# Performance work log

Hardware: AMD Instinct MI355X
Metric: run time of the kernel (lower is better)

The kernel has to match this reference:

```python
import jax, jax.numpy as jnp
import numpy as np

B, T, N, D = 16, 24, 2048, 64
L, K = 2, 3  # num_layers, cheb_k


def setup_inputs() -> dict:
    key = jax.random.key(0)
    ks = jax.random.split(key, 6)
    x = jax.random.normal(ks[0], (B, T, N, D), dtype=jnp.float32)
    init_state = jnp.zeros((L, B, N, D), dtype=jnp.float32)
    adj = jax.random.uniform(ks[1], (N, N), dtype=jnp.float32)
    adj = adj / jnp.sum(adj, axis=-1, keepdims=True)  # row-normalized adjacency
    cin = 2 * D
    Wg = jax.random.normal(ks[2], (L, K, cin, 2 * D), dtype=jnp.float32) * (1.0 / np.sqrt(K * cin))
    bg = jnp.zeros((L, 2 * D), dtype=jnp.float32)
    Wu = jax.random.normal(ks[3], (L, K, cin, D), dtype=jnp.float32) * (1.0 / np.sqrt(K * cin))
    bu = jnp.zeros((L, D), dtype=jnp.float32)
    return {"x": x, "init_state": init_state, "adj_matrix": adj,
            "Wg": Wg, "bg": bg, "Wu": Wu, "bu": bu}


def _cheb_supports(adj, k):
    # T0=I, T1=A, Tk = 2*A@T_{k-1} - T_{k-2}
    n = adj.shape[0]
    sup = [jnp.eye(n, dtype=adj.dtype), adj]
    for _ in range(2, k):
        sup.append(2.0 * adj @ sup[-1] - sup[-2])
    return jnp.stack(sup[:k], axis=0)  # [K, N, N]


def _gconv(xs, supports, W, b):
    # xs: [B,N,Cin], supports: [K,N,N], W: [K,Cin,Cout]
    xg = jnp.einsum('knm,bmc->bknc', supports, xs)
    return jnp.einsum('bknc,kco->bno', xg, W) + b


def _cell(x_t, state, supports, Wg_l, bg_l, Wu_l, bu_l):
    ins = jnp.concatenate([x_t, state], axis=-1)  # [B,N,2D]
    zr = jax.nn.sigmoid(_gconv(ins, supports, Wg_l, bg_l))
    z, r = jnp.split(zr, 2, axis=-1)
    cand_in = jnp.concatenate([x_t, z * state], axis=-1)
    hc = jnp.tanh(_gconv(cand_in, supports, Wu_l, bu_l))
    return r * state + (1.0 - r) * hc


def reference(x, init_state, adj_matrix, Wg, bg, Wu, bu):
    supports = _cheb_supports(adj_matrix, K)
    current = x  # [B,T,N,D]
    hiddens = []
    for l in range(L):
        def step(state, x_t, l=l):
            new = _cell(x_t, state, supports, Wg[l], bg[l], Wu[l], bu[l])
            return new, new
        last, seq = jax.lax.scan(step, init_state[l], jnp.swapaxes(current, 0, 1))
        hiddens.append(last)
        current = x + jnp.swapaxes(seq, 0, 1)  # residual over the stacked states
    return current, jnp.stack(hiddens, axis=0)
```

## Files before the change

### kernel.cpp

```cpp
#include <hip/hip_runtime.h>
#include <hip/hip_bf16.h>
#include <math.h>

typedef __bf16 bf16x8 __attribute__((ext_vector_type(8)));
typedef float f32x4 __attribute__((ext_vector_type(4)));
typedef __hip_bfloat16 bf16s;

constexpr int kB = 16, kT = 24, kN = 2048, kD = 64;
constexpr size_t kBND = (size_t)kB * kN * kD;

struct Slot { const void* p0; const void* p1; int astr0, trow0, astr1, trow1, type; };
struct Slots6 { Slot s[6]; };
struct DiffGrp { const bf16s* src; bf16s* oA; bf16s* oA2; };
struct DiffP { const bf16s* S0; const bf16s* S1; DiffGrp g[4]; int colsPerGrp; };

__device__ __forceinline__ void async_copy16(void* lds, const void* g) {
  __builtin_amdgcn_global_load_lds((const __attribute__((address_space(1))) void*)g,
                                   (__attribute__((address_space(3))) void*)lds,
                                   16, 0, 0);
}


__device__ __forceinline__ void diff_core(
    const bf16s* __restrict__ S, const bf16s* __restrict__ Bsrc,
    int m0, int c0, bf16s* lA, bf16s* lB, f32x4 (&acc)[4][4])
{
  const int tid = threadIdx.x, lane = tid & 63, wave = tid >> 6;
  const int wm = (wave >> 1) * 64, wn = (wave & 1) * 64;
  const f32x4 zero = {0.f, 0.f, 0.f, 0.f};
#pragma unroll
  for (int i = 0; i < 4; ++i)
#pragma unroll
    for (int j = 0; j < 4; ++j) acc[i][j] = zero;

  const int ra = tid >> 3;
  const int cs = ((tid & 7) ^ (ra & 7)) * 8;
  const int rk0 = ((lane >> 4) ^ (lane & 7)) * 8;
  const int rk1 = ((4 + (lane >> 4)) ^ (lane & 7)) * 8;

  for (int k0 = 0; k0 < 2048; k0 += 64) {
#pragma unroll
    for (int i = 0; i < 4; ++i) {
      async_copy16(lA + (size_t)(i * 256 + tid) * 8,
                   S + (size_t)(m0 + i * 32 + ra) * 2048 + k0 + cs);
      async_copy16(lB + (size_t)(i * 256 + tid) * 8,
                   Bsrc + (size_t)(c0 + i * 32 + ra) * 2048 + k0 + cs);
    }
    __syncthreads();
#pragma unroll
    for (int ks = 0; ks < 2; ++ks) {
      const int rk = ks ? rk1 : rk0;
      bf16x8 av[4], bv[4];
#pragma unroll
      for (int f = 0; f < 4; ++f) {
        av[f] = *(const bf16x8*)(lA + (size_t)(wm + f * 16 + (lane & 15)) * 64 + rk);
        bv[f] = *(const bf16x8*)(lB + (size_t)(wn + f * 16 + (lane & 15)) * 64 + rk);
      }
#pragma unroll
      for (int i = 0; i < 4; ++i)
#pragma unroll
        for (int j = 0; j < 4; ++j)
          acc[i][j] = __builtin_amdgcn_mfma_f32_16x16x32_bf16(av[i], bv[j], acc[i][j], 0, 0, 0);
    }
    __syncthreads();
  }
}

__global__ __launch_bounds__(256) void k_diff(DiffP p)
{
  __shared__ bf16s lA[128 * 64];
  __shared__ bf16s lB[128 * 64];
  const int mi = blockIdx.x;
  const bf16s* S = (mi >> 4) ? p.S1 : p.S0;
  const int m0 = (mi & 15) * 128;
  const int ybpg = p.colsPerGrp >> 7;
  const int grp = blockIdx.y / ybpg;
  const int c0 = (blockIdx.y - grp * ybpg) * 128;
  const DiffGrp G = p.g[grp];

  f32x4 acc[4][4];
  diff_core(S, G.src, m0, c0, lA, lB, acc);

  bf16s* out = (mi >> 4) ? G.oA2 : G.oA;
  const int lane = threadIdx.x & 63, wave = threadIdx.x >> 6;
  const int wm = (wave >> 1) * 64, wn = (wave & 1) * 64;
  const int rq = (lane >> 4) * 4, cl = lane & 15;
#pragma unroll
  for (int fm = 0; fm < 4; ++fm)
#pragma unroll
    for (int fn = 0; fn < 4; ++fn)
#pragma unroll
      for (int q = 0; q < 4; ++q) {
        int gm = m0 + wm + fm * 16 + rq + q;
        int gc = c0 + wn + fn * 16 + cl;
        size_t off = ((size_t)(gc >> 6) * 2048 + gm) * 64 + (gc & 63);
        out[off] = __float2bfloat16(acc[fm][fn][q]);
      }
}

__global__ __launch_bounds__(256) void k_a2(
    const bf16s* __restrict__ A, const bf16s* __restrict__ AT, bf16s* A2)
{
  __shared__ bf16s lA[128 * 64];
  __shared__ bf16s lB[128 * 64];
  const int m0 = blockIdx.x * 128, n0 = blockIdx.y * 128;
  f32x4 acc[4][4];
  diff_core(A, AT, m0, n0, lA, lB, acc);
  const int lane = threadIdx.x & 63, wave = threadIdx.x >> 6;
  const int wm = (wave >> 1) * 64, wn = (wave & 1) * 64;
  const int rq = (lane >> 4) * 4, cl = lane & 15;
#pragma unroll
  for (int fm = 0; fm < 4; ++fm)
#pragma unroll
    for (int fn = 0; fn < 4; ++fn)
#pragma unroll
      for (int q = 0; q < 4; ++q) {
        int gm = m0 + wm + fm * 16 + rq + q;
        int gc = n0 + wn + fn * 16 + cl;
        A2[(size_t)gm * 2048 + gc] = __float2bfloat16(2.f * acc[fm][fn][q] - (gm == gc ? 1.f : 0.f));
      }
}

template<int BN>
__device__ __forceinline__ void small_core(
    const Slots6& sl, int m0, const bf16s* __restrict__ W,
    bf16s* lA, bf16s* lB, f32x4 (&acc)[4][BN / 32])
{
  const int tid = threadIdx.x, lane = tid & 63, wave = tid >> 6;
  const int wm = (wave >> 1) * 64, wn = (wave & 1) * (BN / 2);
  const f32x4 zero = {0.f, 0.f, 0.f, 0.f};
#pragma unroll
  for (int i = 0; i < 4; ++i)
#pragma unroll
    for (int j = 0; j < BN / 32; ++j) acc[i][j] = zero;

  const int ra = tid >> 3;
  const int cs = ((tid & 7) ^ (ra & 7)) * 8;
  const int rk0 = ((lane >> 4) ^ (lane & 7)) * 8;
  const int rk1 = ((4 + (lane >> 4)) ^ (lane & 7)) * 8;

#pragma unroll
  for (int ks = 0; ks < 6; ++ks) {
    const Slot sd = sl.s[ks];
    if (sd.type == 0) {
      const bf16s* base = (const bf16s*)sd.p0;
#pragma unroll
      for (int i = 0; i < 4; ++i) {
        int row = m0 + i * 32 + ra;
        size_t roff = ((size_t)(row >> 11) * sd.astr0 + sd.trow0 + (row & 2047)) * 64 + cs;
        async_copy16(lA + (size_t)(i * 256 + tid) * 8, base + roff);
      }
    } else if (sd.type == 1) {
#pragma unroll
      for (int i = 0; i < 4; ++i) {
        int row = m0 + i * 32 + ra;
        size_t roff = ((size_t)(row >> 11) * sd.astr0 + sd.trow0 + (row & 2047)) * 64 + cs;
        const float4* q0 = (const float4*)((const float*)sd.p0 + roff);
        float4 a = q0[0], b = q0[1];
        union { bf16x8 v; bf16s h[8]; } u;
        u.h[0] = __float2bfloat16(a.x); u.h[1] = __float2bfloat16(a.y);
        u.h[2] = __float2bfloat16(a.z); u.h[3] = __float2bfloat16(a.w);
        u.h[4] = __float2bfloat16(b.x); u.h[5] = __float2bfloat16(b.y);
        u.h[6] = __float2bfloat16(b.z); u.h[7] = __float2bfloat16(b.w);
        *(bf16x8*)(lA + (size_t)(i * 256 + tid) * 8) = u.v;
      }
    } else {
#pragma unroll
      for (int i = 0; i < 4; ++i) {
        int row = m0 + i * 32 + ra;
        size_t r0o = ((size_t)(row >> 11) * sd.astr0 + sd.trow0 + (row & 2047)) * 64 + cs;
        size_t r1o = ((size_t)(row >> 11) * sd.astr1 + sd.trow1 + (row & 2047)) * 64 + cs;
        union { bf16x8 v; bf16s h[8]; } a, b, o;
        a.v = *(const bf16x8*)((const bf16s*)sd.p0 + r0o);
        b.v = *(const bf16x8*)((const bf16s*)sd.p1 + r1o);
#pragma unroll
        for (int j = 0; j < 8; ++j)
          o.h[j] = __float2bfloat16(__bfloat162float(a.h[j]) + __bfloat162float(b.h[j]));
        *(bf16x8*)(lA + (size_t)(i * 256 + tid) * 8) = o.v;
      }
    }
#pragma unroll
    for (int i = 0; i < BN / 32; ++i)
      async_copy16(lB + (size_t)(i * 256 + tid) * 8,
                   W + (size_t)(i * 32 + ra) * 384 + ks * 64 + cs);
    __syncthreads();
#pragma unroll
    for (int kss = 0; kss < 2; ++kss) {
      const int rk = kss ? rk1 : rk0;
      bf16x8 av[4], bv[BN / 32];
#pragma unroll
      for (int f = 0; f < 4; ++f)
        av[f] = *(const bf16x8*)(lA + (size_t)(wm + f * 16 + (lane & 15)) * 64 + rk);
#pragma unroll
      for (int f = 0; f < BN / 32; ++f)
        bv[f] = *(const bf16x8*)(lB + (size_t)(wn + f * 16 + (lane & 15)) * 64 + rk);
#pragma unroll
      for (int i = 0; i < 4; ++i)
#pragma unroll
        for (int j = 0; j < BN / 32; ++j)
          acc[i][j] = __builtin_amdgcn_mfma_f32_16x16x32_bf16(av[i], bv[j], acc[i][j], 0, 0, 0);
    }
    __syncthreads();
  }
}

struct LayerG {
  Slots6 sl; const bf16s* W; const float* bias;
  const float* h; bf16s* zh; bf16s* zhT; float* r;
};
__global__ __launch_bounds__(256) void k_gate(LayerG A, LayerG B, int nA)
{
  __shared__ bf16s lA[128 * 64];
  __shared__ bf16s lB[128 * 64];
  const int bx = blockIdx.x;
  const bool isA = bx < nA;
  const LayerG L = isA ? A : B;
  const int m0 = (isA ? bx : bx - nA) * 128;
  f32x4 acc[4][4];
  small_core<128>(L.sl, m0, L.W, lA, lB, acc);
  const int lane = threadIdx.x & 63, wave = threadIdx.x >> 6;
  const int wm = (wave >> 1) * 64, wn = (wave & 1) * 64;
  const int rq = (lane >> 4) * 4, cl = lane & 15;
#pragma unroll
  for (int fm = 0; fm < 4; ++fm)
#pragma unroll
    for (int fn = 0; fn < 4; ++fn) {
      const int o = wn + fn * 16 + cl;
      const float bias = L.bias[o];
#pragma unroll
      for (int q = 0; q < 4; ++q) {
        size_t gm = (size_t)m0 + wm + fm * 16 + rq + q;
        float s = 1.f / (1.f + expf(-(acc[fm][fn][q] + bias)));
        if (o < 64) {
          float zh = s * L.h[gm * 64 + o];
          L.zh[gm * 64 + o] = __float2bfloat16(zh);
          L.zhT[((size_t)((gm >> 11) * 64 + o)) * 2048 + (gm & 2047)] = __float2bfloat16(zh);
        } else {
          L.r[gm * 64 + (o - 64)] = s;
        }
      }
    }
}

struct LayerC {
  Slots6 sl; const bf16s* W; const float* bias;
  const float* r; float* h32; bf16s* hT; bf16s* h_bf; float* hid;
  bf16s* x1;
  float* outC;
  const float* x0; int t;
};
__global__ __launch_bounds__(256) void k_cand(LayerC A, LayerC B, int nA)
{
  __shared__ bf16s lA[128 * 64];
  __shared__ bf16s lB[64 * 64];
  const int bx = blockIdx.x;
  const bool isA = bx < nA;
  const LayerC L = isA ? A : B;
  const int m0 = (isA ? bx : bx - nA) * 128;
  f32x4 acc[4][2];
  small_core<64>(L.sl, m0, L.W, lA, lB, acc);
  const int lane = threadIdx.x & 63, wave = threadIdx.x >> 6;
  const int wm = (wave >> 1) * 64, wn = (wave & 1) * 32;
  const int rq = (lane >> 4) * 4, cl = lane & 15;
#pragma unroll
  for (int fm = 0; fm < 4; ++fm)
#pragma unroll
    for (int fn = 0; fn < 2; ++fn) {
      const int d = wn + fn * 16 + cl;
      const float bias = L.bias[d];
#pragma unroll
      for (int q = 0; q < 4; ++q) {
        size_t gm = (size_t)m0 + wm + fm * 16 + rq + q;
        float hc = tanhf(acc[fm][fn][q] + bias);
        float r = L.r[gm * 64 + d];
        float h = L.h32[gm * 64 + d];
        float hn = r * h + (1.f - r) * hc;
        L.h32[gm * 64 + d] = hn;
        int b = (int)(gm >> 11), n = (int)(gm & 2047);
        L.hT[((size_t)(b * 64 + d)) * 2048 + n] = __float2bfloat16(hn);
        L.h_bf[gm * 64 + d] = __float2bfloat16(hn);
        size_t xi = (((size_t)b * kT + L.t) * 2048 + n) * 64 + d;
        if (L.x1) L.x1[gm * 64 + d] = __float2bfloat16(L.x0[xi] + hn);
        if (L.outC) L.outC[xi] = L.x0[xi] + hn;
        if (L.hid) L.hid[gm * 64 + d] = hn;
      }
    }
}

__global__ __launch_bounds__(256) void transpose_cvt(
    const float* in, bf16s* out, int nrows, int ncols,
    size_t in_ostride, size_t out_ostride)
{
  __shared__ float tile[64][65];
  const int r0 = blockIdx.x * 64, c0 = blockIdx.y * 64;
  in  += (size_t)blockIdx.z * in_ostride;
  out += (size_t)blockIdx.z * out_ostride;
  const int tx = threadIdx.x & 63, ty = threadIdx.x >> 6;
#pragma unroll
  for (int i = 0; i < 64; i += 4)
    tile[ty + i][tx] = in[(size_t)(r0 + ty + i) * ncols + c0 + tx];
  __syncthreads();
#pragma unroll
  for (int i = 0; i < 64; i += 4)
    out[(size_t)(c0 + ty + i) * nrows + r0 + tx] = __float2bfloat16(tile[tx][ty + i]);
}

__global__ __launch_bounds__(256) void k_cvt(const float* in, bf16s* out, int n)
{
  int i = blockIdx.x * 256 + threadIdx.x;
  if (i < n) out[i] = __float2bfloat16(in[i]);
}

__global__ __launch_bounds__(256) void k_repack(
    const float* Wg, const float* Wu, bf16s* WgT, bf16s* WuT)
{
  int idx = blockIdx.x * 256 + threadIdx.x;
  if (idx < 2 * 3 * 128 * 128) {
    int o = idx & 127, cin = (idx >> 7) & 127, k = (idx >> 14) % 3, l = idx / 49152;
    WgT[((size_t)(l * 128 + o)) * 384 + (2 * k + (cin >> 6)) * 64 + (cin & 63)] =
        __float2bfloat16(Wg[idx]);
  }
  if (idx < 2 * 3 * 128 * 64) {
    int o = idx & 63, cin = (idx >> 6) & 127, k = (idx >> 13) % 3, l = idx / 24576;
    WuT[((size_t)(l * 64 + o)) * 384 + (2 * k + (cin >> 6)) * 64 + (cin & 63)] =
        __float2bfloat16(Wu[idx]);
  }
}

__global__ __launch_bounds__(256) void init_layer(
    const float* ist_l, float* h32, bf16s* hT, bf16s* h_bf)
{
  size_t idx = (size_t)blockIdx.x * 256 + threadIdx.x;
  if (idx >= kBND) return;
  int d = (int)(idx & 63);
  size_t row = idx >> 6;
  int n = (int)(row & 2047), b = (int)(row >> 11);
  float h = ist_l[idx];
  h32[idx] = h;
  hT[((size_t)(b * 64 + d)) * 2048 + n] = __float2bfloat16(h);
  h_bf[idx] = __float2bfloat16(h);
}

extern "C" void kernel_launch(void* const* d_in, const int* in_sizes, int n_in,
                              void* d_out, int out_size, void* d_ws, size_t ws_size,
                              hipStream_t stream)
{
  (void)in_sizes; (void)n_in; (void)out_size; (void)ws_size;
  const float* x   = (const float*)d_in[0];
  const float* ist = (const float*)d_in[1];
  const float* adj = (const float*)d_in[2];
  const float* Wg  = (const float*)d_in[3];
  const float* bg  = (const float*)d_in[4];
  const float* Wu  = (const float*)d_in[5];
  const float* bu  = (const float*)d_in[6];
  float* outCur = (float*)d_out;
  float* outHid = outCur + (size_t)kB * kT * kN * kD;

  char* p = (char*)d_ws;
  auto carve = [&](size_t bytes) { char* q = p; p += (bytes + 255) & ~(size_t)255; return q; };
  bf16s* A_bf  = (bf16s*)carve((size_t)2048 * 2048 * 2);
  bf16s* A2_bf = (bf16s*)carve((size_t)2048 * 2048 * 2);
  bf16s* WgT   = (bf16s*)carve((size_t)2 * 128 * 384 * 2);
  bf16s* WuT   = (bf16s*)carve((size_t)2 * 64 * 384 * 2);
  float* h32b  = (float*)carve(2 * kBND * 4);
  float* r32b  = (float*)carve(2 * kBND * 4);
  bf16s* hTb   = (bf16s*)carve(2 * kBND * 2);
  bf16s* hbfb  = (bf16s*)carve(2 * kBND * 2);
  bf16s* zhTb  = (bf16s*)carve(2 * kBND * 2);
  bf16s* zhbfb = (bf16s*)carve(2 * kBND * 2);
  bf16s* x1b   = (bf16s*)carve(2 * kBND * 2);
  bf16s* sAh0  = (bf16s*)carve(kBND * 2);
  bf16s* sA2h0 = (bf16s*)carve(kBND * 2);
  bf16s* sAh1  = (bf16s*)carve(kBND * 2);
  bf16s* sA2h1 = (bf16s*)carve(kBND * 2);
  bf16s* sZ0   = (bf16s*)carve(kBND * 2);
  bf16s* sA2Z0 = (bf16s*)carve(kBND * 2);
  bf16s* sZ1   = (bf16s*)carve(kBND * 2);
  bf16s* sA2Z1 = (bf16s*)carve(kBND * 2);
  const size_t xTfull = (size_t)kB * kT * kD * kN * 2;
  bf16s* AxF  = (bf16s*)carve(xTfull);
  bf16s* A2xF = (bf16s*)carve(xTfull);
  bf16s* xTh  = (bf16s*)carve(xTfull / 2);
  bf16s* AT_bf = AxF;

  float* h32_0 = h32b;   float* h32_1 = h32b + kBND;
  float* r32_0 = r32b;   float* r32_1 = r32b + kBND;
  bf16s* hT0 = hTb;      bf16s* hT1 = hTb + kBND;
  bf16s* hbf0 = hbfb;    bf16s* hbf1 = hbfb + kBND;
  bf16s* zhT0 = zhTb;    bf16s* zhT1 = zhTb + kBND;
  bf16s* zhbf0 = zhbfb;  bf16s* zhbf1 = zhbfb + kBND;

  k_cvt<<<dim3((2048 * 2048 + 255) / 256), 256, 0, stream>>>(adj, A_bf, 2048 * 2048);
  transpose_cvt<<<dim3(32, 32, 1), 256, 0, stream>>>(adj, AT_bf, 2048, 2048, 0, 0);
  k_a2<<<dim3(16, 16, 1), 256, 0, stream>>>(A_bf, AT_bf, A2_bf);
  k_repack<<<dim3(384), 256, 0, stream>>>(Wg, Wu, WgT, WuT);
  init_layer<<<dim3((int)(kBND / 256)), 256, 0, stream>>>(ist, h32_0, hT0, hbf0);
  init_layer<<<dim3((int)(kBND / 256)), 256, 0, stream>>>(ist + kBND, h32_1, hT1, hbf1);

  for (int h = 0; h < 2; ++h) {
    size_t off = (size_t)h * 8 * kT * 131072;
    transpose_cvt<<<dim3(32, 1, 8 * kT), 256, 0, stream>>>(x + off, xTh, 2048, 64, 131072, 131072);
    DiffP dp; dp.S0 = A_bf; dp.S1 = A2_bf; dp.colsPerGrp = 12288;
    dp.g[0] = DiffGrp{xTh, AxF + off, A2xF + off};
    dp.g[1] = dp.g[2] = dp.g[3] = DiffGrp{nullptr, nullptr, nullptr};
    k_diff<<<dim3(32, 96), 256, 0, stream>>>(dp);
  }

  auto Sb = [](const void* p0, int astr, int trow) {
    return Slot{p0, nullptr, astr, trow, 0, 0, 0};
  };
  auto Sf = [](const void* p0, int astr, int trow) {
    return Slot{p0, nullptr, astr, trow, 0, 0, 1};
  };
  auto S2 = [](const void* p0, const void* p1, int astr1, int trow1) {
    return Slot{p0, p1, 2048, 0, astr1, trow1, 2};
  };

  for (int s = 0; s <= kT; ++s) {
    const bool aA = (s < kT), aB = (s >= 1);
    const int tA = s, tB = s - 1;
    const int nA = aA ? 256 : 0, nB = aB ? 256 : 0;
    bf16s* x1cur = x1b + (size_t)(s & 1) * kBND;
    bf16s* x1prev = x1b + (size_t)((s - 1) & 1) * kBND;

    {
      DiffP dp; dp.S0 = A_bf; dp.S1 = A2_bf; dp.colsPerGrp = 1024;
      int ng = 0;
      dp.g[ng++] = DiffGrp{hT0, sAh0, sA2h0};
      if (aB) dp.g[ng++] = DiffGrp{hT1, sAh1, sA2h1};
      for (int i = ng; i < 4; ++i) dp.g[i] = DiffGrp{nullptr, nullptr, nullptr};
      k_diff<<<dim3(32, 8 * ng), 256, 0, stream>>>(dp);
    }

    {
      LayerG GA = {}, GB = {};
      if (aA) {
        GA.sl.s[0] = Sf(x, kT * 2048, tA * 2048);
        GA.sl.s[1] = Sb(hbf0, 2048, 0);
        GA.sl.s[2] = Sb(AxF, kT * 2048, tA * 2048);
        GA.sl.s[3] = Sb(sAh0, 2048, 0);
        GA.sl.s[4] = Sb(A2xF, kT * 2048, tA * 2048);
        GA.sl.s[5] = Sb(sA2h0, 2048, 0);
        GA.W = WgT; GA.bias = bg; GA.h = h32_0; GA.zh = zhbf0; GA.zhT = zhT0; GA.r = r32_0;
      }
      if (aB) {
        GB.sl.s[0] = Sb(x1prev, 2048, 0);
        GB.sl.s[1] = Sb(hbf1, 2048, 0);
        GB.sl.s[2] = S2(sAh0, AxF, kT * 2048, tB * 2048);
        GB.sl.s[3] = Sb(sAh1, 2048, 0);
        GB.sl.s[4] = S2(sA2h0, A2xF, kT * 2048, tB * 2048);
        GB.sl.s[5] = Sb(sA2h1, 2048, 0);
        GB.W = WgT + (size_t)128 * 384; GB.bias = bg + 128;
        GB.h = h32_1; GB.zh = zhbf1; GB.zhT = zhT1; GB.r = r32_1;
      }
      k_gate<<<dim3(nA + nB), 256, 0, stream>>>(GA, GB, nA);
    }

    {
      DiffP dp; dp.S0 = A_bf; dp.S1 = A2_bf; dp.colsPerGrp = 1024;
      int ng = 0;
      if (aA) dp.g[ng++] = DiffGrp{zhT0, sZ0, sA2Z0};
      if (aB) dp.g[ng++] = DiffGrp{zhT1, sZ1, sA2Z1};
      for (int i = ng; i < 4; ++i) dp.g[i] = DiffGrp{nullptr, nullptr, nullptr};
      k_diff<<<dim3(32, 8 * ng), 256, 0, stream>>>(dp);
    }

    {
      LayerC CA = {}, CB = {};
      if (aA) {
        CA.sl.s[0] = Sf(x, kT * 2048, tA * 2048);
        CA.sl.s[1] = Sb(zhbf0, 2048, 0);
        CA.sl.s[2] = Sb(AxF, kT * 2048, tA * 2048);
        CA.sl.s[3] = Sb(sZ0, 2048, 0);
        CA.sl.s[4] = Sb(A2xF, kT * 2048, tA * 2048);
        CA.sl.s[5] = Sb(sA2Z0, 2048, 0);
        CA.W = WuT; CA.bias = bu; CA.r = r32_0; CA.h32 = h32_0; CA.hT = hT0; CA.h_bf = hbf0;
        CA.hid = (tA == kT - 1) ? outHid : nullptr;
        CA.x1 = x1cur; CA.outC = nullptr; CA.x0 = x; CA.t = tA;
      }
      if (aB) {
        CB.sl.s[0] = Sb(x1prev, 2048, 0);
        CB.sl.s[1] = Sb(zhbf1, 2048, 0);
        CB.sl.s[2] = S2(sAh0, AxF, kT * 2048, tB * 2048);
        CB.sl.s[3] = Sb(sZ1, 2048, 0);
        CB.sl.s[4] = S2(sA2h0, A2xF, kT * 2048, tB * 2048);
        CB.sl.s[5] = Sb(sA2Z1, 2048, 0);
        CB.W = WuT + (size_t)64 * 384; CB.bias = bu + 64;
        CB.r = r32_1; CB.h32 = h32_1; CB.hT = hT1; CB.h_bf = hbf1;
        CB.hid = (tB == kT - 1) ? outHid + kBND : nullptr;
        CB.x1 = nullptr; CB.outC = outCur; CB.x0 = x; CB.t = tB;
      }
      k_cand<<<dim3(nA + nB), 256, 0, stream>>>(CA, CB, nA);
    }
  }
}
```

Baseline: 5.091 ms.

## Replace per-step kernel launches with one persistent cooperative kernel using grid syncs

Moves the whole 25-step recurrence (diffusion, gate, diffusion, candidate phases) into one cooperative persistent kernel that separates phases with grid.sync, removing about 100 kernel launches. The diffusion tiles are also reordered with a swizzle so consecutive blocks share the same support rows, for better L2 reuse. The old multi-launch path is kept as a fallback if the cooperative launch fails. Risks include the cost of grid-wide barriers, occupancy limits from the 2-blocks-per-CU launch bound with larger LDS in the candidate phase, and weaker load balancing than hardware scheduling.

Result: slower. 10.66 ms (+109.4%).

```diff
diff --git a/kernel.cpp b/kernel.cpp
--- a/kernel.cpp
+++ b/kernel.cpp
@@ -1,6 +1,9 @@
 #include <hip/hip_runtime.h>
 #include <hip/hip_bf16.h>
+#include <hip/hip_cooperative_groups.h>
 #include <math.h>
+
+namespace cg = cooperative_groups;
 
 typedef __bf16 bf16x8 __attribute__((ext_vector_type(8)));
 typedef float f32x4 __attribute__((ext_vector_type(4)));
@@ -64,6 +67,28 @@
     }
     __syncthreads();
   }
+}
+
+__device__ __forceinline__ void diff_tile(
+    const bf16s* __restrict__ S, const bf16s* __restrict__ src, bf16s* out,
+    int m0, int c0, bf16s* lA, bf16s* lB)
+{
+  f32x4 acc[4][4];
+  diff_core(S, src, m0, c0, lA, lB, acc);
+  const int lane = threadIdx.x & 63, wave = threadIdx.x >> 6;
+  const int wm = (wave >> 1) * 64, wn = (wave & 1) * 64;
+  const int rq = (lane >> 4) * 4, cl = lane & 15;
+#pragma unroll
+  for (int fm = 0; fm < 4; ++fm)
+#pragma unroll
+    for (int fn = 0; fn < 4; ++fn)
+#pragma unroll
+      for (int q = 0; q < 4; ++q) {
+        int gm = m0 + wm + fm * 16 + rq + q;
+        int gc = c0 + wn + fn * 16 + cl;
+        size_t off = ((size_t)(gc >> 6) * 2048 + gm) * 64 + (gc & 63);
+        out[off] = __float2bfloat16(acc[fm][fn][q]);
+      }
 }
 
 __global__ __launch_bounds__(256) void k_diff(DiffP p)
@@ -77,25 +102,8 @@
   const int grp = blockIdx.y / ybpg;
   const int c0 = (blockIdx.y - grp * ybpg) * 128;
   const DiffGrp G = p.g[grp];
-
-  f32x4 acc[4][4];
-  diff_core(S, G.src, m0, c0, lA, lB, acc);
-
   bf16s* out = (mi >> 4) ? G.oA2 : G.oA;
-  const int lane = threadIdx.x & 63, wave = threadIdx.x >> 6;
-  const int wm = (wave >> 1) * 64, wn = (wave & 1) * 64;
-  const int rq = (lane >> 4) * 4, cl = lane & 15;
-#pragma unroll
-  for (int fm = 0; fm < 4; ++fm)
-#pragma unroll
-    for (int fn = 0; fn < 4; ++fn)
-#pragma unroll
-      for (int q = 0; q < 4; ++q) {
-        int gm = m0 + wm + fm * 16 + rq + q;
-        int gc = c0 + wn + fn * 16 + cl;
-        size_t off = ((size_t)(gc >> 6) * 2048 + gm) * 64 + (gc & 63);
-        out[off] = __float2bfloat16(acc[fm][fn][q]);
-      }
+  diff_tile(S, G.src, out, m0, c0, lA, lB);
 }
 
 __global__ __launch_bounds__(256) void k_a2(
@@ -208,14 +216,8 @@
   Slots6 sl; const bf16s* W; const float* bias;
   const float* h; bf16s* zh; bf16s* zhT; float* r;
 };
-__global__ __launch_bounds__(256) void k_gate(LayerG A, LayerG B, int nA)
-{
-  __shared__ bf16s lA[128 * 64];
-  __shared__ bf16s lB[128 * 64];
-  const int bx = blockIdx.x;
-  const bool isA = bx < nA;
-  const LayerG L = isA ? A : B;
-  const int m0 = (isA ? bx : bx - nA) * 128;
+__device__ __forceinline__ void gate_tile(const LayerG& L, int m0, bf16s* lA, bf16s* lB)
+{
   f32x4 acc[4][4];
   small_core<128>(L.sl, m0, L.W, lA, lB, acc);
   const int lane = threadIdx.x & 63, wave = threadIdx.x >> 6;
@@ -245,18 +247,10 @@
 struct LayerC {
   Slots6 sl; const bf16s* W; const float* bias;
   const float* r; float* h32; bf16s* hT; bf16s* h_bf; float* hid;
-  bf16s* x1;
-  float* outC;
-  const float* x0; int t;
+  bf16s* x1; float* outC; const float* x0; int t;
 };
-__global__ __launch_bounds__(256) void k_cand(LayerC A, LayerC B, int nA)
-{
-  __shared__ bf16s lA[128 * 64];
-  __shared__ bf16s lB[64 * 64];
-  const int bx = blockIdx.x;
-  const bool isA = bx < nA;
-  const LayerC L = isA ? A : B;
-  const int m0 = (isA ? bx : bx - nA) * 128;
+__device__ __forceinline__ void cand_tile(const LayerC& L, int m0, bf16s* lA, bf16s* lB)
+{
   f32x4 acc[4][2];
   small_core<64>(L.sl, m0, L.W, lA, lB, acc);
   const int lane = threadIdx.x & 63, wave = threadIdx.x >> 6;
@@ -285,6 +279,154 @@
         if (L.hid) L.hid[gm * 64 + d] = hn;
       }
     }
+}
+
+__device__ __forceinline__ Slot Sb_d(const void* p0, int astr, int trow) {
+  return Slot{p0, nullptr, astr, trow, 0, 0, 0};
+}
+__device__ __forceinline__ Slot Sf_d(const void* p0, int astr, int trow) {
+  return Slot{p0, nullptr, astr, trow, 0, 0, 1};
+}
+__device__ __forceinline__ Slot S2_d(const void* p0, const void* p1, int astr1, int trow1) {
+  return Slot{p0, p1, 2048, 0, astr1, trow1, 2};
+}
+
+__global__ __launch_bounds__(256) void k_gate(LayerG A, LayerG B, int nA)
+{
+  __shared__ bf16s lA[128 * 64];
+  __shared__ bf16s lB[128 * 64];
+  const int bx = blockIdx.x;
+  const bool isA = bx < nA;
+  const LayerG L = isA ? A : B;
+  gate_tile(L, (isA ? bx : bx - nA) * 128, lA, lB);
+}
+
+__global__ __launch_bounds__(256) void k_cand(LayerC A, LayerC B, int nA)
+{
+  __shared__ bf16s lA[128 * 64];
+  __shared__ bf16s lB[128 * 64];
+  const int bx = blockIdx.x;
+  const bool isA = bx < nA;
+  const LayerC L = isA ? A : B;
+  cand_tile(L, (isA ? bx : bx - nA) * 128, lA, lB);
+}
+
+struct SuperP {
+  const bf16s *A, *A2, *AxF, *A2xF;
+  const float *x;
+  const bf16s *WgT, *WuT; const float *bg, *bu;
+  float *h32_0, *h32_1, *r32_0, *r32_1;
+  bf16s *hT0, *hT1, *hbf0, *hbf1;
+  bf16s *zhT0, *zhT1, *zhbf0, *zhbf1;
+  bf16s *x1b;
+  bf16s *sAh0, *sA2h0, *sAh1, *sA2h1, *sZ0, *sA2Z0, *sZ1, *sA2Z1;
+  float *outCur, *outHid;
+};
+
+__device__ __forceinline__ int swz_tile(int b, int nt) {
+  return (nt >= 512) ? (((b & 7) << 6) | (b >> 3)) : (((b & 7) << 5) | (b >> 3));
+}
+
+__global__ __launch_bounds__(256, 2) void k_super(SuperP P)
+{
+  __shared__ bf16s lA[128 * 64];
+  __shared__ bf16s lB[128 * 64];
+  cg::grid_group grid = cg::this_grid();
+  const int bid = blockIdx.x;
+  const int nb = gridDim.x;
+
+  for (int s = 0; s <= kT; ++s) {
+    const bool aA = (s < kT), aB = (s >= 1);
+    const int tA = s, tB = s - 1;
+    bf16s* x1cur  = P.x1b + (size_t)(s & 1) * kBND;
+    bf16s* x1prev = P.x1b + (size_t)((s - 1) & 1) * kBND;
+
+    {
+      const int nt = aB ? 512 : 256;
+      for (int b = bid; b < nt; b += nb) {
+        const int t = swz_tile(b, nt);
+        const int g = t >> 8, r = t & 255;
+        const bf16s* S = (r >> 7) ? P.A2 : P.A;
+        const bf16s* src = g ? P.hT1 : P.hT0;
+        bf16s* out = g ? ((r >> 7) ? P.sA2h1 : P.sAh1) : ((r >> 7) ? P.sA2h0 : P.sAh0);
+        diff_tile(S, src, out, ((r >> 3) & 15) * 128, (r & 7) * 128, lA, lB);
+      }
+    }
+    grid.sync();
+
+    for (int b = bid; b < 512; b += nb) {
+      const bool lyr1 = (b >= 256);
+      if (lyr1 ? !aB : !aA) continue;
+      LayerG L;
+      if (!lyr1) {
+        L.sl.s[0] = Sf_d(P.x, kT * 2048, tA * 2048);
+        L.sl.s[1] = Sb_d(P.hbf0, 2048, 0);
+        L.sl.s[2] = Sb_d(P.AxF, kT * 2048, tA * 2048);
+        L.sl.s[3] = Sb_d(P.sAh0, 2048, 0);
+        L.sl.s[4] = Sb_d(P.A2xF, kT * 2048, tA * 2048);
+        L.sl.s[5] = Sb_d(P.sA2h0, 2048, 0);
+        L.W = P.WgT; L.bias = P.bg; L.h = P.h32_0;
+        L.zh = P.zhbf0; L.zhT = P.zhT0; L.r = P.r32_0;
+      } else {
+        L.sl.s[0] = Sb_d(x1prev, 2048, 0);
+        L.sl.s[1] = Sb_d(P.hbf1, 2048, 0);
+        L.sl.s[2] = S2_d(P.sAh0, P.AxF, kT * 2048, tB * 2048);
+        L.sl.s[3] = Sb_d(P.sAh1, 2048, 0);
+        L.sl.s[4] = S2_d(P.sA2h0, P.A2xF, kT * 2048, tB * 2048);
+        L.sl.s[5] = Sb_d(P.sA2h1, 2048, 0);
+        L.W = P.WgT + (size_t)128 * 384; L.bias = P.bg + 128; L.h = P.h32_1;
+        L.zh = P.zhbf1; L.zhT = P.zhT1; L.r = P.r32_1;
+      }
+      gate_tile(L, (b & 255) * 128, lA, lB);
+    }
+    grid.sync();
+
+    {
+      const int ng1 = (aA ? 1 : 0) + (aB ? 1 : 0);
+      const int nt = 256 * ng1;
+      for (int b = bid; b < nt; b += nb) {
+        const int t = swz_tile(b, nt);
+        const int g = (ng1 == 2) ? (t >> 8) : (aA ? 0 : 1);
+        const int r = t & 255;
+        const bf16s* S = (r >> 7) ? P.A2 : P.A;
+        const bf16s* src = g ? P.zhT1 : P.zhT0;
+        bf16s* out = g ? ((r >> 7) ? P.sA2Z1 : P.sZ1) : ((r >> 7) ? P.sA2Z0 : P.sZ0);
+        diff_tile(S, src, out, ((r >> 3) & 15) * 128, (r & 7) * 128, lA, lB);
+      }
+    }
+    grid.sync();
+
+    for (int b = bid; b < 512; b += nb) {
+      const bool lyr1 = (b >= 256);
+      if (lyr1 ? !aB : !aA) continue;
+      LayerC L;
+      if (!lyr1) {
+        L.sl.s[0] = Sf_d(P.x, kT * 2048, tA * 2048);
+        L.sl.s[1] = Sb_d(P.zhbf0, 2048, 0);
+        L.sl.s[2] = Sb_d(P.AxF, kT * 2048, tA * 2048);
+        L.sl.s[3] = Sb_d(P.sZ0, 2048, 0);
+        L.sl.s[4] = Sb_d(P.A2xF, kT * 2048, tA * 2048);
+        L.sl.s[5] = Sb_d(P.sA2Z0, 2048, 0);
+        L.W = P.WuT; L.bias = P.bu; L.r = P.r32_0; L.h32 = P.h32_0;
+        L.hT = P.hT0; L.h_bf = P.hbf0;
+        L.hid = (tA == kT - 1) ? P.outHid : nullptr;
+        L.x1 = x1cur; L.outC = nullptr; L.x0 = P.x; L.t = tA;
+      } else {
+        L.sl.s[0] = Sb_d(x1prev, 2048, 0);
+        L.sl.s[1] = Sb_d(P.zhbf1, 2048, 0);
+        L.sl.s[2] = S2_d(P.sAh0, P.AxF, kT * 2048, tB * 2048);
+        L.sl.s[3] = Sb_d(P.sZ1, 2048, 0);
+        L.sl.s[4] = S2_d(P.sA2h0, P.A2xF, kT * 2048, tB * 2048);
+        L.sl.s[5] = Sb_d(P.sA2Z1, 2048, 0);
+        L.W = P.WuT + (size_t)64 * 384; L.bias = P.bu + 64; L.r = P.r32_1; L.h32 = P.h32_1;
+        L.hT = P.hT1; L.h_bf = P.hbf1;
+        L.hid = (tB == kT - 1) ? P.outHid + kBND : nullptr;
+        L.x1 = nullptr; L.outC = P.outCur; L.x0 = P.x; L.t = tB;
+      }
+      cand_tile(L, (b & 255) * 128, lA, lB);
+    }
+    grid.sync();
+  }
 }
 
 __global__ __launch_bounds__(256) void transpose_cvt(
@@ -383,19 +525,12 @@
   bf16s* xTh  = (bf16s*)carve(xTfull / 2);
   bf16s* AT_bf = AxF;
 
-  float* h32_0 = h32b;   float* h32_1 = h32b + kBND;
-  float* r32_0 = r32b;   float* r32_1 = r32b + kBND;
-  bf16s* hT0 = hTb;      bf16s* hT1 = hTb + kBND;
-  bf16s* hbf0 = hbfb;    bf16s* hbf1 = hbfb + kBND;
-  bf16s* zhT0 = zhTb;    bf16s* zhT1 = zhTb + kBND;
-  bf16s* zhbf0 = zhbfb;  bf16s* zhbf1 = zhbfb + kBND;
-
   k_cvt<<<dim3((2048 * 2048 + 255) / 256), 256, 0, stream>>>(adj, A_bf, 2048 * 2048);
   transpose_cvt<<<dim3(32, 32, 1), 256, 0, stream>>>(adj, AT_bf, 2048, 2048, 0, 0);
   k_a2<<<dim3(16, 16, 1), 256, 0, stream>>>(A_bf, AT_bf, A2_bf);
   k_repack<<<dim3(384), 256, 0, stream>>>(Wg, Wu, WgT, WuT);
-  init_layer<<<dim3((int)(kBND / 256)), 256, 0, stream>>>(ist, h32_0, hT0, hbf0);
-  init_layer<<<dim3((int)(kBND / 256)), 256, 0, stream>>>(ist + kBND, h32_1, hT1, hbf1);
+  init_layer<<<dim3((int)(kBND / 256)), 256, 0, stream>>>(ist, h32b, hTb, hbfb);
+  init_layer<<<dim3((int)(kBND / 256)), 256, 0, stream>>>(ist + kBND, h32b + kBND, hTb + kBND, hbfb + kBND);
 
   for (int h = 0; h < 2; ++h) {
     size_t off = (size_t)h * 8 * kT * 131072;
@@ -406,91 +541,103 @@
     k_diff<<<dim3(32, 96), 256, 0, stream>>>(dp);
   }
 
-  auto Sb = [](const void* p0, int astr, int trow) {
-    return Slot{p0, nullptr, astr, trow, 0, 0, 0};
-  };
-  auto Sf = [](const void* p0, int astr, int trow) {
-    return Slot{p0, nullptr, astr, trow, 0, 0, 1};
-  };
-  auto S2 = [](const void* p0, const void* p1, int astr1, int trow1) {
-    return Slot{p0, p1, 2048, 0, astr1, trow1, 2};
-  };
-
-  for (int s = 0; s <= kT; ++s) {
-    const bool aA = (s < kT), aB = (s >= 1);
-    const int tA = s, tB = s - 1;
-    const int nA = aA ? 256 : 0, nB = aB ? 256 : 0;
-    bf16s* x1cur = x1b + (size_t)(s & 1) * kBND;
-    bf16s* x1prev = x1b + (size_t)((s - 1) & 1) * kBND;
-
-    {
-      DiffP dp; dp.S0 = A_bf; dp.S1 = A2_bf; dp.colsPerGrp = 1024;
-      int ng = 0;
-      dp.g[ng++] = DiffGrp{hT0, sAh0, sA2h0};
-      if (aB) dp.g[ng++] = DiffGrp{hT1, sAh1, sA2h1};
-      for (int i = ng; i < 4; ++i) dp.g[i] = DiffGrp{nullptr, nullptr, nullptr};
-      k_diff<<<dim3(32, 8 * ng), 256, 0, stream>>>(dp);
-    }
-
-    {
-      LayerG GA = {}, GB = {};
-      if (aA) {
-        GA.sl.s[0] = Sf(x, kT * 2048, tA * 2048);
-        GA.sl.s[1] = Sb(hbf0, 2048, 0);
-        GA.sl.s[2] = Sb(AxF, kT * 2048, tA * 2048);
-        GA.sl.s[3] = Sb(sAh0, 2048, 0);
-        GA.sl.s[4] = Sb(A2xF, kT * 2048, tA * 2048);
-        GA.sl.s[5] = Sb(sA2h0, 2048, 0);
-        GA.W = WgT; GA.bias = bg; GA.h = h32_0; GA.zh = zhbf0; GA.zhT = zhT0; GA.r = r32_0;
-      }
-      if (aB) {
-        GB.sl.s[0] = Sb(x1prev, 2048, 0);
-        GB.sl.s[1] = Sb(hbf1, 2048, 0);
-        GB.sl.s[2] = S2(sAh0, AxF, kT * 2048, tB * 2048);
-        GB.sl.s[3] = Sb(sAh1, 2048, 0);
-        GB.sl.s[4] = S2(sA2h0, A2xF, kT * 2048, tB * 2048);
-        GB.sl.s[5] = Sb(sA2h1, 2048, 0);
-        GB.W = WgT + (size_t)128 * 384; GB.bias = bg + 128;
-        GB.h = h32_1; GB.zh = zhbf1; GB.zhT = zhT1; GB.r = r32_1;
-      }
-      k_gate<<<dim3(nA + nB), 256, 0, stream>>>(GA, GB, nA);
-    }
-
-    {
-      DiffP dp; dp.S0 = A_bf; dp.S1 = A2_bf; dp.colsPerGrp = 1024;
-      int ng = 0;
-      if (aA) dp.g[ng++] = DiffGrp{zhT0, sZ0, sA2Z0};
-      if (aB) dp.g[ng++] = DiffGrp{zhT1, sZ1, sA2Z1};
-      for (int i = ng; i < 4; ++i) dp.g[i] = DiffGrp{nullptr, nullptr, nullptr};
-      k_diff<<<dim3(32, 8 * ng), 256, 0, stream>>>(dp);
-    }
-
-    {
-      LayerC CA = {}, CB = {};
-      if (aA) {
-        CA.sl.s[0] = Sf(x, kT * 2048, tA * 2048);
-        CA.sl.s[1] = Sb(zhbf0, 2048, 0);
-        CA.sl.s[2] = Sb(AxF, kT * 2048, tA * 2048);
-        CA.sl.s[3] = Sb(sZ0, 2048, 0);
-        CA.sl.s[4] = Sb(A2xF, kT * 2048, tA * 2048);
-        CA.sl.s[5] = Sb(sA2Z0, 2048, 0);
-        CA.W = WuT; CA.bias = bu; CA.r = r32_0; CA.h32 = h32_0; CA.hT = hT0; CA.h_bf = hbf0;
-        CA.hid = (tA == kT - 1) ? outHid : nullptr;
-        CA.x1 = x1cur; CA.outC = nullptr; CA.x0 = x; CA.t = tA;
-      }
-      if (aB) {
-        CB.sl.s[0] = Sb(x1prev, 2048, 0);
-        CB.sl.s[1] = Sb(zhbf1, 2048, 0);
-        CB.sl.s[2] = S2(sAh0, AxF, kT * 2048, tB * 2048);
-        CB.sl.s[3] = Sb(sZ1, 2048, 0);
-        CB.sl.s[4] = S2(sA2h0, A2xF, kT * 2048, tB * 2048);
-        CB.sl.s[5] = Sb(sA2Z1, 2048, 0);
-        CB.W = WuT + (size_t)64 * 384; CB.bias = bu + 64;
-        CB.r = r32_1; CB.h32 = h32_1; CB.hT = hT1; CB.h_bf = hbf1;
-        CB.hid = (tB == kT - 1) ? outHid + kBND : nullptr;
-        CB.x1 = nullptr; CB.outC = outCur; CB.x0 = x; CB.t = tB;
-      }
-      k_cand<<<dim3(nA + nB), 256, 0, stream>>>(CA, CB, nA);
+  SuperP P;
+  P.A = A_bf; P.A2 = A2_bf; P.AxF = AxF; P.A2xF = A2xF;
+  P.x = x; P.WgT = WgT; P.WuT = WuT; P.bg = bg; P.bu = bu;
+  P.h32_0 = h32b; P.h32_1 = h32b + kBND;
+  P.r32_0 = r32b; P.r32_1 = r32b + kBND;
+  P.hT0 = hTb; P.hT1 = hTb + kBND;
+  P.hbf0 = hbfb; P.hbf1 = hbfb + kBND;
+  P.zhT0 = zhTb; P.zhT1 = zhTb + kBND;
+  P.zhbf0 = zhbfb; P.zhbf1 = zhbfb + kBND;
+  P.x1b = x1b;
+  P.sAh0 = sAh0; P.sA2h0 = sA2h0; P.sAh1 = sAh1; P.sA2h1 = sA2h1;
+  P.sZ0 = sZ0; P.sA2Z0 = sA2Z0; P.sZ1 = sZ1; P.sA2Z1 = sA2Z1;
+  P.outCur = outCur; P.outHid = outHid;
+  void* args[] = { &P };
+  hipError_t ce = hipLaunchCooperativeKernel((void*)k_super, dim3(512), dim3(256), args, 0, stream);
+  if (ce != hipSuccess)
+    ce = hipLaunchCooperativeKernel((void*)k_super, dim3(256), dim3(256), args, 0, stream);
+
+  if (ce != hipSuccess) {
+    auto Sb = [](const void* p0, int astr, int trow) { return Slot{p0, nullptr, astr, trow, 0, 0, 0}; };
+    auto Sf = [](const void* p0, int astr, int trow) { return Slot{p0, nullptr, astr, trow, 0, 0, 1}; };
+    auto S2 = [](const void* p0, const void* p1, int astr1, int trow1) {
+      return Slot{p0, p1, 2048, 0, astr1, trow1, 2};
+    };
+    for (int s = 0; s <= kT; ++s) {
+      const bool aA = (s < kT), aB = (s >= 1);
+      const int tA = s, tB = s - 1;
+      const int nA = aA ? 256 : 0, nB = aB ? 256 : 0;
+      bf16s* x1cur  = x1b + (size_t)(s & 1) * kBND;
+      bf16s* x1prev = x1b + (size_t)((s - 1) & 1) * kBND;
+
+      {
+        DiffP dp; dp.S0 = A_bf; dp.S1 = A2_bf; dp.colsPerGrp = 1024;
+        int ng = 0;
+        dp.g[ng++] = DiffGrp{hTb, sAh0, sA2h0};
+        if (aB) dp.g[ng++] = DiffGrp{hTb + kBND, sAh1, sA2h1};
+        for (int i = ng; i < 4; ++i) dp.g[i] = DiffGrp{nullptr, nullptr, nullptr};
+        k_diff<<<dim3(32, 8 * ng), 256, 0, stream>>>(dp);
+      }
+      {
+        LayerG GA = {}, GB = {};
+        if (aA) {
+          GA.sl.s[0] = Sf(x, kT * 2048, tA * 2048);
+          GA.sl.s[1] = Sb(hbfb, 2048, 0);
+          GA.sl.s[2] = Sb(AxF, kT * 2048, tA * 2048);
+          GA.sl.s[3] = Sb(sAh0, 2048, 0);
+          GA.sl.s[4] = Sb(A2xF, kT * 2048, tA * 2048);
+          GA.sl.s[5] = Sb(sA2h0, 2048, 0);
+          GA.W = WgT; GA.bias = bg; GA.h = h32b; GA.zh = zhbfb; GA.zhT = zhTb; GA.r = r32b;
+        }
+        if (aB) {
+          GB.sl.s[0] = Sb(x1prev, 2048, 0);
+          GB.sl.s[1] = Sb(hbfb + kBND, 2048, 0);
+          GB.sl.s[2] = S2(sAh0, AxF, kT * 2048, tB * 2048);
+          GB.sl.s[3] = Sb(sAh1, 2048, 0);
+          GB.sl.s[4] = S2(sA2h0, A2xF, kT * 2048, tB * 2048);
+          GB.sl.s[5] = Sb(sA2h1, 2048, 0);
+          GB.W = WgT + (size_t)128 * 384; GB.bias = bg + 128;
+          GB.h = h32b + kBND; GB.zh = zhbfb + kBND; GB.zhT = zhTb + kBND; GB.r = r32b + kBND;
+        }
+        k_gate<<<dim3(nA + nB), 256, 0, stream>>>(GA, GB, nA);
+      }
+      {
+        DiffP dp; dp.S0 = A_bf; dp.S1 = A2_bf; dp.colsPerGrp = 1024;
+        int ng = 0;
+        if (aA) dp.g[ng++] = DiffGrp{zhTb, sZ0, sA2Z0};
+        if (aB) dp.g[ng++] = DiffGrp{zhTb + kBND, sZ1, sA2Z1};
+        for (int i = ng; i < 4; ++i) dp.g[i] = DiffGrp{nullptr, nullptr, nullptr};
+        k_diff<<<dim3(32, 8 * ng), 256, 0, stream>>>(dp);
+      }
+      {
+        LayerC CA = {}, CB = {};
+        if (aA) {
+          CA.sl.s[0] = Sf(x, kT * 2048, tA * 2048);
+          CA.sl.s[1] = Sb(zhbfb, 2048, 0);
+          CA.sl.s[2] = Sb(AxF, kT * 2048, tA * 2048);
+          CA.sl.s[3] = Sb(sZ0, 2048, 0);
+          CA.sl.s[4] = Sb(A2xF, kT * 2048, tA * 2048);
+          CA.sl.s[5] = Sb(sA2Z0, 2048, 0);
+          CA.W = WuT; CA.bias = bu; CA.r = r32b; CA.h32 = h32b; CA.hT = hTb; CA.h_bf = hbfb;
+          CA.hid = (tA == kT - 1) ? outHid : nullptr;
+          CA.x1 = x1cur; CA.outC = nullptr; CA.x0 = x; CA.t = tA;
+        }
+        if (aB) {
+          CB.sl.s[0] = Sb(x1prev, 2048, 0);
+          CB.sl.s[1] = Sb(zhbfb + kBND, 2048, 0);
+          CB.sl.s[2] = S2(sAh0, AxF, kT * 2048, tB * 2048);
+          CB.sl.s[3] = Sb(sZ1, 2048, 0);
+          CB.sl.s[4] = S2(sA2h0, A2xF, kT * 2048, tB * 2048);
+          CB.sl.s[5] = Sb(sA2Z1, 2048, 0);
+          CB.W = WuT + (size_t)64 * 384; CB.bias = bu + 64;
+          CB.r = r32b + kBND; CB.h32 = h32b + kBND; CB.hT = hTb + kBND; CB.h_bf = hbfb + kBND;
+          CB.hid = (tB == kT - 1) ? outHid + kBND : nullptr;
+          CB.x1 = nullptr; CB.outC = outCur; CB.x0 = x; CB.t = tB;
+        }
+        k_cand<<<dim3(nA + nB), 256, 0, stream>>>(CA, CB, nA);
+      }
     }
   }
 }
```
